# Optimization experiments

Measured on AMD Instinct MI355X. Metric: run time of the kernel, lower is better.

## Reference

```python
import jax, jax.numpy as jnp
import numpy as np

N, D = 8192, 32
SIGMA = 4.0
DAMPING = 0.5
MAX_ITER = 10
SHIFT_TOL = 1e-4


def _sqdist(a, b):
    # squared euclidean distances, (Na, Nb)
    sq = jnp.sum(a * a, axis=1)[:, None] + jnp.sum(b * b, axis=1)[None, :] - 2.0 * (a @ b.T)
    return jnp.maximum(sq, 0.0)


def setup_inputs() -> dict:
    key = jax.random.key(0)
    x = jax.random.normal(key, (N, D), dtype=jnp.float32)
    sigma = jnp.asarray(SIGMA, dtype=jnp.float32)  # learned scalar nn.Parameter
    return {"x": x, "sigma": sigma}


def _find_centroids(x, sigma):
    gamma = 1.0 / (2.0 * sigma ** 2)

    def body(carry, _):
        centroids, done = carry
        sq = _sqdist(x, centroids)              # (N, N); cdist(x,c)**2
        w = jnp.exp(-sq * gamma)                # gaussian kernel weights
        new_c = (w @ x) / jnp.sum(w, axis=1, keepdims=True)
        shift = jnp.linalg.norm(new_c - centroids, axis=1)
        # torch breaks BEFORE the damping update when max shift < tol
        done_new = done | (jnp.max(shift) < SHIFT_TOL)
        centroids = jnp.where(done_new, centroids,
                              DAMPING * centroids + (1.0 - DAMPING) * new_c)
        return (centroids, done_new), None

    (centroids, _), _ = jax.lax.scan(jax.remat(body), (x, jnp.asarray(False)), None, length=MAX_ITER)
    return centroids


def _nms_keep(x, centroids, threshold):
    n = centroids.shape[0]
    sq_pc = _sqdist(x, centroids)
    closest = jnp.argmin(sq_pc, axis=1)                      # (N,)
    scores = jnp.zeros((n,), jnp.int32).at[closest].add(1)   # counts per centroid
    sq_cc = _sqdist(centroids, centroids)
    overlap = (sq_cc < threshold ** 2) & ~jnp.eye(n, dtype=bool)
    order = jnp.argsort(-scores)                             # descending by score

    def body(keep, idx):
        active = keep[idx]
        keep2 = jnp.where(active, keep & ~overlap[idx], keep)
        keep2 = keep2.at[idx].set(jnp.where(active, scores[idx] > 0, keep2[idx]))
        return keep2, None

    keep, _ = jax.lax.scan(body, jnp.ones((n,), bool), order)
    return keep


def reference(x, sigma):
    centroids = _find_centroids(x, sigma)
    # threshold = sigma.item() in torch -> constant w.r.t. autodiff
    keep = _nms_keep(x, centroids, jax.lax.stop_gradient(sigma))
    # assignment over kept centroids only (dropped centroids get -inf cost -> 0 prob)
    cost = -jnp.sqrt(_sqdist(x, centroids) + 1e-12)
    cost = jnp.where(keep[None, :], cost, -jnp.inf)
    assignment = jax.nn.softmax(cost, axis=1)  # alpha == 1 branch
    return centroids, assignment, keep
```

## Files before the change

### kernel.cpp

```cpp
#include <hip/hip_runtime.h>
#include <math.h>

#define NPTS 8192
#define DIM 32
#define MAX_ITER 10
#define TOL 1e-4f
#define DAMP 0.5f

#define OFF_MSP   0u
#define OFF_CCUR  8650752u
#define OFF_CNEW  8912896u
#define OFF_NX    9175040u
#define OFF_NC    9183232u
#define OFF_PV    9191424u
#define OFF_PJ    9453568u
#define OFF_RKP   9715712u
#define OFF_PM    9977856u
#define OFF_PS   10240000u
#define OFF_MSH  10502144u
#define OFF_SCO  10502208u
#define OFF_ORD  10510400u

__global__ __launch_bounds__(256) void k_init(const float* __restrict__ x,
                                              float* __restrict__ c0,
                                              float* __restrict__ nx,
                                              float* __restrict__ nc) {
    int p = blockIdx.x * blockDim.x + threadIdx.x;
    const float4* xr = (const float4*)(x + (size_t)p * DIM);
    float4* cr = (float4*)(c0 + (size_t)p * DIM);
    float s = 0.f;
#pragma unroll
    for (int q = 0; q < 8; ++q) {
        float4 v = xr[q];
        cr[q] = v;
        s += v.x * v.x + v.y * v.y + v.z * v.z + v.w * v.w;
    }
    nx[p] = s;
    nc[p] = s;
}

__global__ __launch_bounds__(256) void k_ms2(const float* __restrict__ x,
                                             const float* __restrict__ nx,
                                             const float* __restrict__ c,
                                             const float* __restrict__ nc,
                                             const float* __restrict__ sigma_p,
                                             float* __restrict__ P) {
    int t = threadIdx.x;
    int wv = __builtin_amdgcn_readfirstlane(t >> 6);
    int lane = t & 63;
    int it = (int)blockIdx.x >> 5, js = (int)blockIdx.x & 31;
    int i = it * 256 + wv * 64 + lane;

    float sg = sigma_p[0];
    float gamma = 1.f / (2.f * sg * sg);

    float xi[DIM];
    const float4* xr = (const float4*)(x + (size_t)i * DIM);
#pragma unroll
    for (int q = 0; q < 8; ++q) {
        float4 v = xr[q];
        xi[4 * q] = v.x; xi[4 * q + 1] = v.y; xi[4 * q + 2] = v.z; xi[4 * q + 3] = v.w;
    }
    float nxi = nx[i];

    float acc[DIM];
#pragma unroll
    for (int d = 0; d < DIM; ++d) acc[d] = 0.f;
    float wsum = 0.f;

    int j0 = js * 256;
    const float* cb = c + (size_t)j0 * DIM;
    const float* xb = x + (size_t)j0 * DIM;
    const float* ncb = nc + j0;

    for (int jj = 0; jj < 256; ++jj) {
        const float4* cr = (const float4*)(cb + (size_t)jj * DIM);
        const float4* xr2 = (const float4*)(xb + (size_t)jj * DIM);
        float4 C[8], X[8];
#pragma unroll
        for (int q = 0; q < 8; ++q) C[q] = cr[q];
#pragma unroll
        for (int q = 0; q < 8; ++q) X[q] = xr2[q];
        float ncj = ncb[jj];
        float d0 = 0.f, d1 = 0.f, d2 = 0.f, d3 = 0.f;
#pragma unroll
        for (int q = 0; q < 8; ++q) {
            d0 = fmaf(xi[4 * q + 0], C[q].x, d0);
            d1 = fmaf(xi[4 * q + 1], C[q].y, d1);
            d2 = fmaf(xi[4 * q + 2], C[q].z, d2);
            d3 = fmaf(xi[4 * q + 3], C[q].w, d3);
        }
        float sq = fmaxf(nxi + ncj - 2.f * ((d0 + d1) + (d2 + d3)), 0.f);
        float w = __expf(-sq * gamma);
        wsum += w;
#pragma unroll
        for (int q = 0; q < 8; ++q) {
            acc[4 * q + 0] = fmaf(w, X[q].x, acc[4 * q + 0]);
            acc[4 * q + 1] = fmaf(w, X[q].y, acc[4 * q + 1]);
            acc[4 * q + 2] = fmaf(w, X[q].z, acc[4 * q + 2]);
            acc[4 * q + 3] = fmaf(w, X[q].w, acc[4 * q + 3]);
        }
    }

    size_t base = ((size_t)js * 33) * NPTS + i;
#pragma unroll
    for (int d = 0; d < DIM; ++d) P[base + (size_t)d * NPTS] = acc[d];
    P[base + (size_t)32 * NPTS] = wsum;
}

__global__ __launch_bounds__(256) void k_reduce(const float* __restrict__ P,
                                                const float* __restrict__ c_cur,
                                                float* __restrict__ c_new,
                                                unsigned int* __restrict__ maxshift) {
    int i = blockIdx.x * 256 + threadIdx.x;
    float tot[33];
#pragma unroll
    for (int d = 0; d < 33; ++d) tot[d] = 0.f;
    for (int js = 0; js < 32; ++js) {
        size_t base = ((size_t)js * 33) * NPTS + i;
#pragma unroll
        for (int d = 0; d < 33; ++d) tot[d] += P[base + (size_t)d * NPTS];
    }
    float ws = tot[32];
    const float* co = c_cur + (size_t)i * DIM;
    float sh2 = 0.f;
    float ncv[DIM];
#pragma unroll
    for (int d = 0; d < DIM; ++d) {
        float v = tot[d] / ws;
        ncv[d] = v;
        float df = v - co[d];
        sh2 = fmaf(df, df, sh2);
    }
    float4* dst = (float4*)(c_new + (size_t)i * DIM);
#pragma unroll
    for (int q = 0; q < 8; ++q)
        dst[q] = make_float4(ncv[4 * q], ncv[4 * q + 1], ncv[4 * q + 2], ncv[4 * q + 3]);
    atomicMax(maxshift, __float_as_uint(sqrtf(sh2)));
}

__global__ __launch_bounds__(256) void k_update(float* __restrict__ c_cur,
                                                const float* __restrict__ c_new,
                                                float* __restrict__ nc,
                                                const unsigned int* __restrict__ maxshift) {
    if (__uint_as_float(*maxshift) < TOL) return;
    int i = blockIdx.x * 256 + threadIdx.x;
    float4* cc = (float4*)(c_cur + (size_t)i * DIM);
    const float4* cn = (const float4*)(c_new + (size_t)i * DIM);
    float s = 0.f;
#pragma unroll
    for (int q = 0; q < 8; ++q) {
        float4 a = cc[q], b = cn[q];
        float4 r = make_float4(DAMP * a.x + (1.f - DAMP) * b.x,
                               DAMP * a.y + (1.f - DAMP) * b.y,
                               DAMP * a.z + (1.f - DAMP) * b.z,
                               DAMP * a.w + (1.f - DAMP) * b.w);
        cc[q] = r;
        s += r.x * r.x + r.y * r.y + r.z * r.z + r.w * r.w;
    }
    nc[i] = s;
}

__global__ __launch_bounds__(256) void k_scores2(const float* __restrict__ x,
                                                 const float* __restrict__ nx,
                                                 const float* __restrict__ c,
                                                 const float* __restrict__ nc,
                                                 float* __restrict__ pv,
                                                 int* __restrict__ pj) {
    int t = threadIdx.x;
    int wv = __builtin_amdgcn_readfirstlane(t >> 6);
    int lane = t & 63;
    int it = (int)blockIdx.x >> 5, js = (int)blockIdx.x & 31;
    int p = it * 256 + wv * 64 + lane;

    float xi[DIM];
    const float4* xr = (const float4*)(x + (size_t)p * DIM);
#pragma unroll
    for (int q = 0; q < 8; ++q) {
        float4 v = xr[q];
        xi[4 * q] = v.x; xi[4 * q + 1] = v.y; xi[4 * q + 2] = v.z; xi[4 * q + 3] = v.w;
    }
    float nxp = nx[p];

    int j0 = js * 256;
    const float* cb = c + (size_t)j0 * DIM;
    const float* ncb = nc + j0;
    float bestv = INFINITY;
    int bestj = j0;
    for (int jj = 0; jj < 256; ++jj) {
        const float4* cr = (const float4*)(cb + (size_t)jj * DIM);
        float4 C[8];
#pragma unroll
        for (int q = 0; q < 8; ++q) C[q] = cr[q];
        float d0 = 0.f, d1 = 0.f, d2 = 0.f, d3 = 0.f;
#pragma unroll
        for (int q = 0; q < 8; ++q) {
            d0 = fmaf(xi[4 * q + 0], C[q].x, d0);
            d1 = fmaf(xi[4 * q + 1], C[q].y, d1);
            d2 = fmaf(xi[4 * q + 2], C[q].z, d2);
            d3 = fmaf(xi[4 * q + 3], C[q].w, d3);
        }
        float sq = fmaxf(nxp + ncb[jj] - 2.f * ((d0 + d1) + (d2 + d3)), 0.f);
        if (sq < bestv) { bestv = sq; bestj = j0 + jj; }
    }
    pv[(size_t)js * NPTS + p] = bestv;
    pj[(size_t)js * NPTS + p] = bestj;
}

__global__ __launch_bounds__(256) void k_score_comb(const float* __restrict__ pv,
                                                    const int* __restrict__ pj,
                                                    int* __restrict__ scores) {
    int p = blockIdx.x * 256 + threadIdx.x;
    float bv = pv[p];
    int bj = pj[p];
    for (int js = 1; js < 32; ++js) {
        float v = pv[(size_t)js * NPTS + p];
        int j = pj[(size_t)js * NPTS + p];
        if (v < bv) { bv = v; bj = j; }
    }
    atomicAdd(&scores[bj], 1);
}

__global__ __launch_bounds__(256) void k_rank_part(const int* __restrict__ scores,
                                                   int* __restrict__ rkp) {
    int t = threadIdx.x;
    int wv = __builtin_amdgcn_readfirstlane(t >> 6);
    int lane = t & 63;
    int it = (int)blockIdx.x >> 5, js = (int)blockIdx.x & 31;
    int p = it * 256 + wv * 64 + lane;
    int sp = scores[p];
    int j0 = js * 256;
    int r = 0;
    for (int jj = 0; jj < 256; ++jj) {
        int sj = scores[j0 + jj];
        int j = j0 + jj;
        r += (sj > sp) || (sj == sp && j < p);
    }
    rkp[(size_t)js * NPTS + p] = r;
}

__global__ __launch_bounds__(256) void k_rank_comb(const int* __restrict__ rkp,
                                                   int* __restrict__ order) {
    int p = blockIdx.x * 256 + threadIdx.x;
    int r = 0;
    for (int js = 0; js < 32; ++js) r += rkp[(size_t)js * NPTS + p];
    order[r] = p;
}

__global__ __launch_bounds__(1024) void k_nms(const float* __restrict__ c,
                                              const int* __restrict__ order,
                                              const int* __restrict__ scores,
                                              const float* __restrict__ sigma_p,
                                              float* __restrict__ keep_out) {
    __shared__ int s_ord[NPTS];
    __shared__ unsigned char kp[NPTS];
    __shared__ int s_first[16];
    __shared__ int s_next;
    int t = threadIdx.x;
    for (int q = t; q < NPTS; q += 1024) { s_ord[q] = order[q]; kp[q] = 1; }
    __syncthreads();
    float sg = sigma_p[0];
    float thr2 = sg * sg;

    int k = 0;
    while (k < NPTS) {
        int cand = k + t;
        bool hit = (cand < NPTS) && (kp[s_ord[cand]] != 0);
        unsigned long long b = __ballot(hit);
        int wave = t >> 6;
        if ((t & 63) == 0)
            s_first[wave] = b ? (k + (wave << 6) + (__ffsll((unsigned long long)b) - 1))
                              : 0x7fffffff;
        __syncthreads();
        if (t == 0) {
            int mn = s_first[0];
            for (int w2 = 1; w2 < 16; ++w2) mn = min(mn, s_first[w2]);
            s_next = mn;
        }
        __syncthreads();
        int kf = s_next;
        if (kf == 0x7fffffff) { k += 1024; continue; }

        int idx = s_ord[kf];
        float ci[DIM];
        const float4* cr = (const float4*)(c + (size_t)idx * DIM);
#pragma unroll
        for (int q = 0; q < 8; ++q) {
            float4 v = cr[q];
            ci[4 * q] = v.x; ci[4 * q + 1] = v.y; ci[4 * q + 2] = v.z; ci[4 * q + 3] = v.w;
        }
#pragma unroll
        for (int m2 = 0; m2 < 8; ++m2) {
            int j = t + m2 * 1024;
            const float4* cj = (const float4*)(c + (size_t)j * DIM);
            float sq = 0.f;
#pragma unroll
            for (int q = 0; q < 8; ++q) {
                float4 v = cj[q];
                float e0 = v.x - ci[4 * q], e1 = v.y - ci[4 * q + 1];
                float e2 = v.z - ci[4 * q + 2], e3 = v.w - ci[4 * q + 3];
                sq += e0 * e0 + e1 * e1 + e2 * e2 + e3 * e3;
            }
            if (j != idx && sq < thr2) kp[j] = 0;
        }
        __syncthreads();
        if (t == 0) kp[idx] = (scores[idx] > 0) ? 1 : 0;
        __syncthreads();
        k = kf + 1;
    }
    __syncthreads();
    for (int q = t; q < NPTS; q += 1024) keep_out[q] = kp[q] ? 1.0f : 0.0f;
}

__global__ __launch_bounds__(256) void k_apass1(const float* __restrict__ x,
                                                const float* __restrict__ nx,
                                                const float* __restrict__ c,
                                                const float* __restrict__ nc,
                                                const float* __restrict__ keepf,
                                                float* __restrict__ pm,
                                                float* __restrict__ ps) {
    int t = threadIdx.x;
    int wv = __builtin_amdgcn_readfirstlane(t >> 6);
    int lane = t & 63;
    int it = (int)blockIdx.x >> 5, js = (int)blockIdx.x & 31;
    int p = it * 256 + wv * 64 + lane;

    float xi[DIM];
    const float4* xr = (const float4*)(x + (size_t)p * DIM);
#pragma unroll
    for (int q = 0; q < 8; ++q) {
        float4 v = xr[q];
        xi[4 * q] = v.x; xi[4 * q + 1] = v.y; xi[4 * q + 2] = v.z; xi[4 * q + 3] = v.w;
    }
    float nxp = nx[p];

    int j0 = js * 256;
    const float* cb = c + (size_t)j0 * DIM;
    const float* ncb = nc + j0;
    const float* kb = keepf + j0;
    float m = -1e30f, S = 0.f;
    for (int jj = 0; jj < 256; ++jj) {
        const float4* cr = (const float4*)(cb + (size_t)jj * DIM);
        float4 C[8];
#pragma unroll
        for (int q = 0; q < 8; ++q) C[q] = cr[q];
        float d0 = 0.f, d1 = 0.f, d2 = 0.f, d3 = 0.f;
#pragma unroll
        for (int q = 0; q < 8; ++q) {
            d0 = fmaf(xi[4 * q + 0], C[q].x, d0);
            d1 = fmaf(xi[4 * q + 1], C[q].y, d1);
            d2 = fmaf(xi[4 * q + 2], C[q].z, d2);
            d3 = fmaf(xi[4 * q + 3], C[q].w, d3);
        }
        float sq = fmaxf(nxp + ncb[jj] - 2.f * ((d0 + d1) + (d2 + d3)), 0.f);
        float cost = -sqrtf(sq + 1e-12f);
        float ck = (kb[jj] > 0.5f) ? cost : -INFINITY;
        float mn = fmaxf(m, ck);
        S = S * __expf(m - mn) + __expf(ck - mn);
        m = mn;
    }
    pm[(size_t)js * NPTS + p] = m;
    ps[(size_t)js * NPTS + p] = S;
}

__global__ __launch_bounds__(256) void k_acomb(const float* __restrict__ pm,
                                               const float* __restrict__ ps,
                                               const float* __restrict__ nx,
                                               float* __restrict__ A) {
    int p = blockIdx.x * 256 + threadIdx.x;
    float M = -1e30f;
    for (int js = 0; js < 32; ++js) M = fmaxf(M, pm[(size_t)js * NPTS + p]);
    float SS = 0.f;
    for (int js = 0; js < 32; ++js)
        SS += ps[(size_t)js * NPTS + p] * __expf(pm[(size_t)js * NPTS + p] - M);
    float* row = A + (size_t)p * NPTS;
    row[8189] = nx[p];
    row[8190] = M;
    row[8191] = 1.f / SS;
}

__global__ __launch_bounds__(256) void k_apass2(const float* __restrict__ x,
                                                const float* __restrict__ c,
                                                const float* __restrict__ keepf,
                                                float* __restrict__ A) {
    __shared__ float sNX[16], sM[16], sI[16];
    int t = threadIdx.x;
    int wv = __builtin_amdgcn_readfirstlane(t >> 6);
    int lane = t & 63;
    int p0 = blockIdx.x * 16;
    if (t < 16) {
        const float* row = A + (size_t)(p0 + t) * NPTS;
        sNX[t] = row[8189];
        sM[t] = row[8190];
        sI[t] = row[8191];
    }
    __syncthreads();

    for (int ch = wv; ch < 128; ch += 4) {
        int j = ch * 64 + lane;
        float cj[DIM];
        const float4* cr = (const float4*)(c + (size_t)j * DIM);
        float ncj = 0.f;
#pragma unroll
        for (int q = 0; q < 8; ++q) {
            float4 v = cr[q];
            cj[4 * q] = v.x; cj[4 * q + 1] = v.y; cj[4 * q + 2] = v.z; cj[4 * q + 3] = v.w;
            ncj += v.x * v.x + v.y * v.y + v.z * v.z + v.w * v.w;
        }
        float kpj = keepf[j];
        for (int pp = 0; pp < 16; ++pp) {
            const float4* xrow = (const float4*)(x + (size_t)(p0 + pp) * DIM);
            float4 X[8];
#pragma unroll
            for (int q = 0; q < 8; ++q) X[q] = xrow[q];
            float nxp = sNX[pp], M = sM[pp], inv = sI[pp];
            float d0 = 0.f, d1 = 0.f, d2 = 0.f, d3 = 0.f;
#pragma unroll
            for (int q = 0; q < 8; ++q) {
                d0 = fmaf(cj[4 * q + 0], X[q].x, d0);
                d1 = fmaf(cj[4 * q + 1], X[q].y, d1);
                d2 = fmaf(cj[4 * q + 2], X[q].z, d2);
                d3 = fmaf(cj[4 * q + 3], X[q].w, d3);
            }
            float sq = fmaxf(nxp + ncj - 2.f * ((d0 + d1) + (d2 + d3)), 0.f);
            float cost = -sqrtf(sq + 1e-12f);
            float v = (kpj > 0.5f) ? __expf(cost - M) * inv : 0.f;
            A[(size_t)(p0 + pp) * NPTS + j] = v;
        }
    }
}

extern "C" void kernel_launch(void* const* d_in, const int* in_sizes, int n_in,
                              void* d_out, int out_size, void* d_ws, size_t ws_size,
                              hipStream_t stream) {
    const float* x = (const float*)d_in[0];
    const float* sigma = (const float*)d_in[1];

    float* out = (float*)d_out;
    float* OUT_C = out;
    float* A = out + (size_t)NPTS * DIM;
    float* OUT_K = A + (size_t)NPTS * NPTS;

    float* msP = A + OFF_MSP;
    float* c_cur = A + OFF_CCUR;
    float* c_new = A + OFF_CNEW;
    float* nx = A + OFF_NX;
    float* nc = A + OFF_NC;
    float* pv = A + OFF_PV;
    int* pj = (int*)(A + OFF_PJ);
    int* rkp = (int*)(A + OFF_RKP);
    float* pm = A + OFF_PM;
    float* ps = A + OFF_PS;
    unsigned int* maxshift = (unsigned int*)(A + OFF_MSH);
    int* scores = (int*)(A + OFF_SCO);
    int* order = (int*)(A + OFF_ORD);

    k_init<<<NPTS / 256, 256, 0, stream>>>(x, c_cur, nx, nc);
    for (int itr = 0; itr < MAX_ITER; ++itr) {
        hipMemsetAsync(maxshift, 0, sizeof(unsigned int), stream);
        k_ms2<<<1024, 256, 0, stream>>>(x, nx, c_cur, nc, sigma, msP);
        k_reduce<<<NPTS / 256, 256, 0, stream>>>(msP, c_cur, c_new, maxshift);
        k_update<<<NPTS / 256, 256, 0, stream>>>(c_cur, c_new, nc, maxshift);
    }
    hipMemcpyAsync(OUT_C, c_cur, (size_t)NPTS * DIM * sizeof(float),
                   hipMemcpyDeviceToDevice, stream);

    hipMemsetAsync(scores, 0, NPTS * sizeof(int), stream);
    k_scores2<<<1024, 256, 0, stream>>>(x, nx, OUT_C, nc, pv, pj);
    k_score_comb<<<NPTS / 256, 256, 0, stream>>>(pv, pj, scores);
    k_rank_part<<<1024, 256, 0, stream>>>(scores, rkp);
    k_rank_comb<<<NPTS / 256, 256, 0, stream>>>(rkp, order);
    k_nms<<<1, 1024, 0, stream>>>(OUT_C, order, scores, sigma, OUT_K);

    k_apass1<<<1024, 256, 0, stream>>>(x, nx, OUT_C, nc, OUT_K, pm, ps);
    k_acomb<<<NPTS / 256, 256, 0, stream>>>(pm, ps, nx, A);
    k_apass2<<<NPTS / 16, 256, 0, stream>>>(x, OUT_C, OUT_K, A);
}
```

Baseline: 1.888 ms.

## Register-block two points per thread, drop softmax max pass, retile assignment kernel

The mean-shift, argmin and softmax-sum kernels now handle two query points per thread, so each centroid row loaded is reused across two dot products, and grids are halved. The softmax max is dropped because costs are non-positive and bounded, which removes the online rescaling and the k_acomb kernel. The final pass now stages 128 points in shared memory and tiles over 256 centroids per block. Fast exp2, sqrt and rcp intrinsics replace the library calls, and the separate memsets are folded into k_init with a per-iteration maxshift slot. Risks include higher register pressure and possible underflow for far points when no max subtraction is done.

```diff
diff --git a/kernel.cpp b/kernel.cpp
--- a/kernel.cpp
+++ b/kernel.cpp
@@ -6,6 +6,7 @@
 #define MAX_ITER 10
 #define TOL 1e-4f
 #define DAMP 0.5f
+#define LOG2E 1.4426950408889634f
 
 #define OFF_MSP   0u
 #define OFF_CCUR  8650752u
@@ -15,16 +16,16 @@
 #define OFF_PV    9191424u
 #define OFF_PJ    9453568u
 #define OFF_RKP   9715712u
-#define OFF_PM    9977856u
-#define OFF_PS   10240000u
-#define OFF_MSH  10502144u
-#define OFF_SCO  10502208u
-#define OFF_ORD  10510400u
+#define OFF_MSH   9977856u
+#define OFF_SCO   9977872u
+#define OFF_ORD   9986064u
 
 __global__ __launch_bounds__(256) void k_init(const float* __restrict__ x,
                                               float* __restrict__ c0,
                                               float* __restrict__ nx,
-                                              float* __restrict__ nc) {
+                                              float* __restrict__ nc,
+                                              int* __restrict__ scores,
+                                              unsigned int* __restrict__ msh) {
     int p = blockIdx.x * blockDim.x + threadIdx.x;
     const float4* xr = (const float4*)(x + (size_t)p * DIM);
     float4* cr = (float4*)(c0 + (size_t)p * DIM);
@@ -37,75 +38,103 @@
     }
     nx[p] = s;
     nc[p] = s;
-}
-
-__global__ __launch_bounds__(256) void k_ms2(const float* __restrict__ x,
-                                             const float* __restrict__ nx,
-                                             const float* __restrict__ c,
-                                             const float* __restrict__ nc,
-                                             const float* __restrict__ sigma_p,
-                                             float* __restrict__ P) {
+    scores[p] = 0;
+    if (blockIdx.x == 0 && threadIdx.x < 16) msh[threadIdx.x] = 0u;
+}
+
+__global__ __launch_bounds__(256, 2) void k_ms2(const float* __restrict__ x,
+                                                const float* __restrict__ nx,
+                                                const float* __restrict__ c,
+                                                const float* __restrict__ nc,
+                                                const float* __restrict__ sigma_p,
+                                                float* __restrict__ P) {
     int t = threadIdx.x;
     int wv = __builtin_amdgcn_readfirstlane(t >> 6);
     int lane = t & 63;
     int it = (int)blockIdx.x >> 5, js = (int)blockIdx.x & 31;
-    int i = it * 256 + wv * 64 + lane;
+    int i0 = it * 512 + wv * 128 + lane;
+    int i1 = i0 + 64;
 
     float sg = sigma_p[0];
-    float gamma = 1.f / (2.f * sg * sg);
-
-    float xi[DIM];
-    const float4* xr = (const float4*)(x + (size_t)i * DIM);
-#pragma unroll
-    for (int q = 0; q < 8; ++q) {
-        float4 v = xr[q];
-        xi[4 * q] = v.x; xi[4 * q + 1] = v.y; xi[4 * q + 2] = v.z; xi[4 * q + 3] = v.w;
-    }
-    float nxi = nx[i];
-
-    float acc[DIM];
-#pragma unroll
-    for (int d = 0; d < DIM; ++d) acc[d] = 0.f;
-    float wsum = 0.f;
-
-    int j0 = js * 256;
-    const float* cb = c + (size_t)j0 * DIM;
-    const float* xb = x + (size_t)j0 * DIM;
-    const float* ncb = nc + j0;
+    float ng2 = -LOG2E / (2.f * sg * sg);
+
+    float xi0[DIM], xi1[DIM];
+    {
+        const float4* xr0 = (const float4*)(x + (size_t)i0 * DIM);
+        const float4* xr1 = (const float4*)(x + (size_t)i1 * DIM);
+#pragma unroll
+        for (int q = 0; q < 8; ++q) {
+            float4 a = xr0[q], b = xr1[q];
+            xi0[4 * q] = a.x; xi0[4 * q + 1] = a.y; xi0[4 * q + 2] = a.z; xi0[4 * q + 3] = a.w;
+            xi1[4 * q] = b.x; xi1[4 * q + 1] = b.y; xi1[4 * q + 2] = b.z; xi1[4 * q + 3] = b.w;
+        }
+    }
+    float nx0 = nx[i0], nx1 = nx[i1];
+
+    float acc0[DIM], acc1[DIM];
+#pragma unroll
+    for (int d = 0; d < DIM; ++d) { acc0[d] = 0.f; acc1[d] = 0.f; }
+    float ws0 = 0.f, ws1 = 0.f;
+
+    int jb = js * 256;
+    const float* cb = c + (size_t)jb * DIM;
+    const float* xb = x + (size_t)jb * DIM;
+    const float* ncb = nc + jb;
 
     for (int jj = 0; jj < 256; ++jj) {
-        const float4* cr = (const float4*)(cb + (size_t)jj * DIM);
-        const float4* xr2 = (const float4*)(xb + (size_t)jj * DIM);
-        float4 C[8], X[8];
-#pragma unroll
-        for (int q = 0; q < 8; ++q) C[q] = cr[q];
-#pragma unroll
-        for (int q = 0; q < 8; ++q) X[q] = xr2[q];
-        float ncj = ncb[jj];
-        float d0 = 0.f, d1 = 0.f, d2 = 0.f, d3 = 0.f;
-#pragma unroll
-        for (int q = 0; q < 8; ++q) {
-            d0 = fmaf(xi[4 * q + 0], C[q].x, d0);
-            d1 = fmaf(xi[4 * q + 1], C[q].y, d1);
-            d2 = fmaf(xi[4 * q + 2], C[q].z, d2);
-            d3 = fmaf(xi[4 * q + 3], C[q].w, d3);
-        }
-        float sq = fmaxf(nxi + ncj - 2.f * ((d0 + d1) + (d2 + d3)), 0.f);
-        float w = __expf(-sq * gamma);
-        wsum += w;
-#pragma unroll
-        for (int q = 0; q < 8; ++q) {
-            acc[4 * q + 0] = fmaf(w, X[q].x, acc[4 * q + 0]);
-            acc[4 * q + 1] = fmaf(w, X[q].y, acc[4 * q + 1]);
-            acc[4 * q + 2] = fmaf(w, X[q].z, acc[4 * q + 2]);
-            acc[4 * q + 3] = fmaf(w, X[q].w, acc[4 * q + 3]);
-        }
-    }
-
-    size_t base = ((size_t)js * 33) * NPTS + i;
-#pragma unroll
-    for (int d = 0; d < DIM; ++d) P[base + (size_t)d * NPTS] = acc[d];
-    P[base + (size_t)32 * NPTS] = wsum;
+        float w0, w1;
+        {
+            const float4* cr = (const float4*)(cb + (size_t)jj * DIM);
+            float4 C[8];
+#pragma unroll
+            for (int q = 0; q < 8; ++q) C[q] = cr[q];
+            float ncj = ncb[jj];
+            float a0 = 0.f, a1 = 0.f, a2 = 0.f, a3 = 0.f;
+            float b0 = 0.f, b1 = 0.f, b2 = 0.f, b3 = 0.f;
+#pragma unroll
+            for (int q = 0; q < 8; ++q) {
+                a0 = fmaf(xi0[4 * q + 0], C[q].x, a0);
+                a1 = fmaf(xi0[4 * q + 1], C[q].y, a1);
+                a2 = fmaf(xi0[4 * q + 2], C[q].z, a2);
+                a3 = fmaf(xi0[4 * q + 3], C[q].w, a3);
+                b0 = fmaf(xi1[4 * q + 0], C[q].x, b0);
+                b1 = fmaf(xi1[4 * q + 1], C[q].y, b1);
+                b2 = fmaf(xi1[4 * q + 2], C[q].z, b2);
+                b3 = fmaf(xi1[4 * q + 3], C[q].w, b3);
+            }
+            float sq0 = fmaxf(fmaf(-2.f, (a0 + a1) + (a2 + a3), nx0 + ncj), 0.f);
+            float sq1 = fmaxf(fmaf(-2.f, (b0 + b1) + (b2 + b3), nx1 + ncj), 0.f);
+            w0 = __builtin_amdgcn_exp2f(ng2 * sq0);
+            w1 = __builtin_amdgcn_exp2f(ng2 * sq1);
+        }
+        ws0 += w0; ws1 += w1;
+        {
+            const float4* xr2 = (const float4*)(xb + (size_t)jj * DIM);
+            float4 X[8];
+#pragma unroll
+            for (int q = 0; q < 8; ++q) X[q] = xr2[q];
+#pragma unroll
+            for (int q = 0; q < 8; ++q) {
+                acc0[4 * q + 0] = fmaf(w0, X[q].x, acc0[4 * q + 0]);
+                acc0[4 * q + 1] = fmaf(w0, X[q].y, acc0[4 * q + 1]);
+                acc0[4 * q + 2] = fmaf(w0, X[q].z, acc0[4 * q + 2]);
+                acc0[4 * q + 3] = fmaf(w0, X[q].w, acc0[4 * q + 3]);
+                acc1[4 * q + 0] = fmaf(w1, X[q].x, acc1[4 * q + 0]);
+                acc1[4 * q + 1] = fmaf(w1, X[q].y, acc1[4 * q + 1]);
+                acc1[4 * q + 2] = fmaf(w1, X[q].z, acc1[4 * q + 2]);
+                acc1[4 * q + 3] = fmaf(w1, X[q].w, acc1[4 * q + 3]);
+            }
+        }
+    }
+
+    size_t base = ((size_t)js * 33) * NPTS + i0;
+#pragma unroll
+    for (int d = 0; d < DIM; ++d) {
+        P[base + (size_t)d * NPTS] = acc0[d];
+        P[base + (size_t)d * NPTS + 64] = acc1[d];
+    }
+    P[base + (size_t)32 * NPTS] = ws0;
+    P[base + (size_t)32 * NPTS + 64] = ws1;
 }
 
 __global__ __launch_bounds__(256) void k_reduce(const float* __restrict__ P,
@@ -122,12 +151,14 @@
         for (int d = 0; d < 33; ++d) tot[d] += P[base + (size_t)d * NPTS];
     }
     float ws = tot[32];
+    float inv = __builtin_amdgcn_rcpf(ws);
+    inv = inv * (2.f - ws * inv);
     const float* co = c_cur + (size_t)i * DIM;
     float sh2 = 0.f;
     float ncv[DIM];
 #pragma unroll
     for (int d = 0; d < DIM; ++d) {
-        float v = tot[d] / ws;
+        float v = tot[d] * inv;
         ncv[d] = v;
         float df = v - co[d];
         sh2 = fmaf(df, df, sh2);
@@ -136,7 +167,7 @@
 #pragma unroll
     for (int q = 0; q < 8; ++q)
         dst[q] = make_float4(ncv[4 * q], ncv[4 * q + 1], ncv[4 * q + 2], ncv[4 * q + 3]);
-    atomicMax(maxshift, __float_as_uint(sqrtf(sh2)));
+    atomicMax(maxshift, __float_as_uint(__builtin_amdgcn_sqrtf(sh2)));
 }
 
 __global__ __launch_bounds__(256) void k_update(float* __restrict__ c_cur,
@@ -161,50 +192,65 @@
     nc[i] = s;
 }
 
-__global__ __launch_bounds__(256) void k_scores2(const float* __restrict__ x,
-                                                 const float* __restrict__ nx,
-                                                 const float* __restrict__ c,
-                                                 const float* __restrict__ nc,
-                                                 float* __restrict__ pv,
-                                                 int* __restrict__ pj) {
+__global__ __launch_bounds__(256, 2) void k_scores2(const float* __restrict__ x,
+                                                    const float* __restrict__ nx,
+                                                    const float* __restrict__ c,
+                                                    const float* __restrict__ nc,
+                                                    float* __restrict__ pv,
+                                                    int* __restrict__ pj) {
     int t = threadIdx.x;
     int wv = __builtin_amdgcn_readfirstlane(t >> 6);
     int lane = t & 63;
     int it = (int)blockIdx.x >> 5, js = (int)blockIdx.x & 31;
-    int p = it * 256 + wv * 64 + lane;
-
-    float xi[DIM];
-    const float4* xr = (const float4*)(x + (size_t)p * DIM);
-#pragma unroll
-    for (int q = 0; q < 8; ++q) {
-        float4 v = xr[q];
-        xi[4 * q] = v.x; xi[4 * q + 1] = v.y; xi[4 * q + 2] = v.z; xi[4 * q + 3] = v.w;
-    }
-    float nxp = nx[p];
-
-    int j0 = js * 256;
-    const float* cb = c + (size_t)j0 * DIM;
-    const float* ncb = nc + j0;
-    float bestv = INFINITY;
-    int bestj = j0;
+    int p0 = it * 512 + wv * 128 + lane;
+    int p1 = p0 + 64;
+
+    float xi0[DIM], xi1[DIM];
+    {
+        const float4* xr0 = (const float4*)(x + (size_t)p0 * DIM);
+        const float4* xr1 = (const float4*)(x + (size_t)p1 * DIM);
+#pragma unroll
+        for (int q = 0; q < 8; ++q) {
+            float4 a = xr0[q], b = xr1[q];
+            xi0[4 * q] = a.x; xi0[4 * q + 1] = a.y; xi0[4 * q + 2] = a.z; xi0[4 * q + 3] = a.w;
+            xi1[4 * q] = b.x; xi1[4 * q + 1] = b.y; xi1[4 * q + 2] = b.z; xi1[4 * q + 3] = b.w;
+        }
+    }
+    float nxp0 = nx[p0], nxp1 = nx[p1];
+
+    int jb = js * 256;
+    const float* cb = c + (size_t)jb * DIM;
+    const float* ncb = nc + jb;
+    float bv0 = INFINITY, bv1 = INFINITY;
+    int bj0 = jb, bj1 = jb;
     for (int jj = 0; jj < 256; ++jj) {
         const float4* cr = (const float4*)(cb + (size_t)jj * DIM);
         float4 C[8];
 #pragma unroll
         for (int q = 0; q < 8; ++q) C[q] = cr[q];
-        float d0 = 0.f, d1 = 0.f, d2 = 0.f, d3 = 0.f;
-#pragma unroll
-        for (int q = 0; q < 8; ++q) {
-            d0 = fmaf(xi[4 * q + 0], C[q].x, d0);
-            d1 = fmaf(xi[4 * q + 1], C[q].y, d1);
-            d2 = fmaf(xi[4 * q + 2], C[q].z, d2);
-            d3 = fmaf(xi[4 * q + 3], C[q].w, d3);
-        }
-        float sq = fmaxf(nxp + ncb[jj] - 2.f * ((d0 + d1) + (d2 + d3)), 0.f);
-        if (sq < bestv) { bestv = sq; bestj = j0 + jj; }
-    }
-    pv[(size_t)js * NPTS + p] = bestv;
-    pj[(size_t)js * NPTS + p] = bestj;
+        float ncj = ncb[jj];
+        float a0 = 0.f, a1 = 0.f, a2 = 0.f, a3 = 0.f;
+        float b0 = 0.f, b1 = 0.f, b2 = 0.f, b3 = 0.f;
+#pragma unroll
+        for (int q = 0; q < 8; ++q) {
+            a0 = fmaf(xi0[4 * q + 0], C[q].x, a0);
+            a1 = fmaf(xi0[4 * q + 1], C[q].y, a1);
+            a2 = fmaf(xi0[4 * q + 2], C[q].z, a2);
+            a3 = fmaf(xi0[4 * q + 3], C[q].w, a3);
+            b0 = fmaf(xi1[4 * q + 0], C[q].x, b0);
+            b1 = fmaf(xi1[4 * q + 1], C[q].y, b1);
+            b2 = fmaf(xi1[4 * q + 2], C[q].z, b2);
+            b3 = fmaf(xi1[4 * q + 3], C[q].w, b3);
+        }
+        float sq0 = fmaxf(fmaf(-2.f, (a0 + a1) + (a2 + a3), nxp0 + ncj), 0.f);
+        float sq1 = fmaxf(fmaf(-2.f, (b0 + b1) + (b2 + b3), nxp1 + ncj), 0.f);
+        if (sq0 < bv0) { bv0 = sq0; bj0 = jb + jj; }
+        if (sq1 < bv1) { bv1 = sq1; bj1 = jb + jj; }
+    }
+    pv[(size_t)js * NPTS + p0] = bv0;
+    pj[(size_t)js * NPTS + p0] = bj0;
+    pv[(size_t)js * NPTS + p1] = bv1;
+    pj[(size_t)js * NPTS + p1] = bj1;
 }
 
 __global__ __launch_bounds__(256) void k_score_comb(const float* __restrict__ pv,
@@ -312,121 +358,134 @@
     for (int q = t; q < NPTS; q += 1024) keep_out[q] = kp[q] ? 1.0f : 0.0f;
 }
 
-__global__ __launch_bounds__(256) void k_apass1(const float* __restrict__ x,
-                                                const float* __restrict__ nx,
-                                                const float* __restrict__ c,
-                                                const float* __restrict__ nc,
-                                                const float* __restrict__ keepf,
-                                                float* __restrict__ pm,
-                                                float* __restrict__ ps) {
+__global__ __launch_bounds__(256, 2) void k_apass1(const float* __restrict__ x,
+                                                   const float* __restrict__ nx,
+                                                   const float* __restrict__ c,
+                                                   const float* __restrict__ nc,
+                                                   const float* __restrict__ keepf,
+                                                   float* __restrict__ ps) {
     int t = threadIdx.x;
     int wv = __builtin_amdgcn_readfirstlane(t >> 6);
     int lane = t & 63;
     int it = (int)blockIdx.x >> 5, js = (int)blockIdx.x & 31;
-    int p = it * 256 + wv * 64 + lane;
-
-    float xi[DIM];
-    const float4* xr = (const float4*)(x + (size_t)p * DIM);
-#pragma unroll
-    for (int q = 0; q < 8; ++q) {
-        float4 v = xr[q];
-        xi[4 * q] = v.x; xi[4 * q + 1] = v.y; xi[4 * q + 2] = v.z; xi[4 * q + 3] = v.w;
-    }
-    float nxp = nx[p];
-
-    int j0 = js * 256;
-    const float* cb = c + (size_t)j0 * DIM;
-    const float* ncb = nc + j0;
-    const float* kb = keepf + j0;
-    float m = -1e30f, S = 0.f;
+    int p0 = it * 512 + wv * 128 + lane;
+    int p1 = p0 + 64;
+
+    float xi0[DIM], xi1[DIM];
+    {
+        const float4* xr0 = (const float4*)(x + (size_t)p0 * DIM);
+        const float4* xr1 = (const float4*)(x + (size_t)p1 * DIM);
+#pragma unroll
+        for (int q = 0; q < 8; ++q) {
+            float4 a = xr0[q], b = xr1[q];
+            xi0[4 * q] = a.x; xi0[4 * q + 1] = a.y; xi0[4 * q + 2] = a.z; xi0[4 * q + 3] = a.w;
+            xi1[4 * q] = b.x; xi1[4 * q + 1] = b.y; xi1[4 * q + 2] = b.z; xi1[4 * q + 3] = b.w;
+        }
+    }
+    float nxp0 = nx[p0], nxp1 = nx[p1];
+
+    int jb = js * 256;
+    const float* cb = c + (size_t)jb * DIM;
+    const float* ncb = nc + jb;
+    const float* kb = keepf + jb;
+    float S0 = 0.f, S1 = 0.f;
     for (int jj = 0; jj < 256; ++jj) {
         const float4* cr = (const float4*)(cb + (size_t)jj * DIM);
         float4 C[8];
 #pragma unroll
         for (int q = 0; q < 8; ++q) C[q] = cr[q];
-        float d0 = 0.f, d1 = 0.f, d2 = 0.f, d3 = 0.f;
-#pragma unroll
-        for (int q = 0; q < 8; ++q) {
-            d0 = fmaf(xi[4 * q + 0], C[q].x, d0);
-            d1 = fmaf(xi[4 * q + 1], C[q].y, d1);
-            d2 = fmaf(xi[4 * q + 2], C[q].z, d2);
-            d3 = fmaf(xi[4 * q + 3], C[q].w, d3);
-        }
-        float sq = fmaxf(nxp + ncb[jj] - 2.f * ((d0 + d1) + (d2 + d3)), 0.f);
-        float cost = -sqrtf(sq + 1e-12f);
-        float ck = (kb[jj] > 0.5f) ? cost : -INFINITY;
-        float mn = fmaxf(m, ck);
-        S = S * __expf(m - mn) + __expf(ck - mn);
-        m = mn;
-    }
-    pm[(size_t)js * NPTS + p] = m;
-    ps[(size_t)js * NPTS + p] = S;
-}
-
-__global__ __launch_bounds__(256) void k_acomb(const float* __restrict__ pm,
-                                               const float* __restrict__ ps,
-                                               const float* __restrict__ nx,
-                                               float* __restrict__ A) {
-    int p = blockIdx.x * 256 + threadIdx.x;
-    float M = -1e30f;
-    for (int js = 0; js < 32; ++js) M = fmaxf(M, pm[(size_t)js * NPTS + p]);
-    float SS = 0.f;
-    for (int js = 0; js < 32; ++js)
-        SS += ps[(size_t)js * NPTS + p] * __expf(pm[(size_t)js * NPTS + p] - M);
-    float* row = A + (size_t)p * NPTS;
-    row[8189] = nx[p];
-    row[8190] = M;
-    row[8191] = 1.f / SS;
-}
-
-__global__ __launch_bounds__(256) void k_apass2(const float* __restrict__ x,
-                                                const float* __restrict__ c,
-                                                const float* __restrict__ keepf,
-                                                float* __restrict__ A) {
-    __shared__ float sNX[16], sM[16], sI[16];
+        float ncj = ncb[jj];
+        float kadd = (kb[jj] > 0.5f) ? 0.f : -1e38f;
+        float a0 = 0.f, a1 = 0.f, a2 = 0.f, a3 = 0.f;
+        float b0 = 0.f, b1 = 0.f, b2 = 0.f, b3 = 0.f;
+#pragma unroll
+        for (int q = 0; q < 8; ++q) {
+            a0 = fmaf(xi0[4 * q + 0], C[q].x, a0);
+            a1 = fmaf(xi0[4 * q + 1], C[q].y, a1);
+            a2 = fmaf(xi0[4 * q + 2], C[q].z, a2);
+            a3 = fmaf(xi0[4 * q + 3], C[q].w, a3);
+            b0 = fmaf(xi1[4 * q + 0], C[q].x, b0);
+            b1 = fmaf(xi1[4 * q + 1], C[q].y, b1);
+            b2 = fmaf(xi1[4 * q + 2], C[q].z, b2);
+            b3 = fmaf(xi1[4 * q + 3], C[q].w, b3);
+        }
+        float sq0 = fmaxf(fmaf(-2.f, (a0 + a1) + (a2 + a3), nxp0 + ncj), 0.f);
+        float sq1 = fmaxf(fmaf(-2.f, (b0 + b1) + (b2 + b3), nxp1 + ncj), 0.f);
+        float r0 = __builtin_amdgcn_sqrtf(sq0 + 1e-12f);
+        float r1 = __builtin_amdgcn_sqrtf(sq1 + 1e-12f);
+        S0 += __builtin_amdgcn_exp2f(fmaf(r0, -LOG2E, kadd));
+        S1 += __builtin_amdgcn_exp2f(fmaf(r1, -LOG2E, kadd));
+    }
+    ps[(size_t)js * NPTS + p0] = S0;
+    ps[(size_t)js * NPTS + p1] = S1;
+}
+
+__global__ __launch_bounds__(256, 4) void k_apass2(const float* __restrict__ x,
+                                                   const float* __restrict__ c,
+                                                   const float* __restrict__ keepf,
+                                                   const float* __restrict__ ps,
+                                                   float* __restrict__ A) {
+    __shared__ float sx[128 * 36];
+    __shared__ float snx[128];
+    __shared__ float sscale[128];
+    __shared__ float spart[256];
     int t = threadIdx.x;
     int wv = __builtin_amdgcn_readfirstlane(t >> 6);
     int lane = t & 63;
-    int p0 = blockIdx.x * 16;
-    if (t < 16) {
-        const float* row = A + (size_t)(p0 + t) * NPTS;
-        sNX[t] = row[8189];
-        sM[t] = row[8190];
-        sI[t] = row[8191];
+    int pt = (int)blockIdx.x >> 5, jt = (int)blockIdx.x & 31;
+    int p0 = pt * 128, j0 = jt * 256;
+
+    {
+        const float4* src = (const float4*)(x + (size_t)p0 * DIM) + t * 4;
+        int row = t >> 1, colh = (t & 1) * 16;
+        float4* dst = (float4*)(sx + row * 36 + colh);
+        float s = 0.f;
+#pragma unroll
+        for (int q = 0; q < 4; ++q) {
+            float4 v = src[q];
+            dst[q] = v;
+            s += v.x * v.x + v.y * v.y + v.z * v.z + v.w * v.w;
+        }
+        spart[t] = s;
     }
     __syncthreads();
-
-    for (int ch = wv; ch < 128; ch += 4) {
-        int j = ch * 64 + lane;
-        float cj[DIM];
+    if (t < 128) {
+        snx[t] = spart[2 * t] + spart[2 * t + 1];
+        float SS = 0.f;
+        for (int js = 0; js < 32; ++js) SS += ps[(size_t)js * NPTS + p0 + t];
+        sscale[t] = 1.f / SS;
+    }
+
+    int j = j0 + wv * 64 + lane;
+    float cj[DIM];
+    float ncj = 0.f;
+    {
         const float4* cr = (const float4*)(c + (size_t)j * DIM);
-        float ncj = 0.f;
 #pragma unroll
         for (int q = 0; q < 8; ++q) {
             float4 v = cr[q];
             cj[4 * q] = v.x; cj[4 * q + 1] = v.y; cj[4 * q + 2] = v.z; cj[4 * q + 3] = v.w;
             ncj += v.x * v.x + v.y * v.y + v.z * v.z + v.w * v.w;
         }
-        float kpj = keepf[j];
-        for (int pp = 0; pp < 16; ++pp) {
-            const float4* xrow = (const float4*)(x + (size_t)(p0 + pp) * DIM);
-            float4 X[8];
-#pragma unroll
-            for (int q = 0; q < 8; ++q) X[q] = xrow[q];
-            float nxp = sNX[pp], M = sM[pp], inv = sI[pp];
-            float d0 = 0.f, d1 = 0.f, d2 = 0.f, d3 = 0.f;
-#pragma unroll
-            for (int q = 0; q < 8; ++q) {
-                d0 = fmaf(cj[4 * q + 0], X[q].x, d0);
-                d1 = fmaf(cj[4 * q + 1], X[q].y, d1);
-                d2 = fmaf(cj[4 * q + 2], X[q].z, d2);
-                d3 = fmaf(cj[4 * q + 3], X[q].w, d3);
-            }
-            float sq = fmaxf(nxp + ncj - 2.f * ((d0 + d1) + (d2 + d3)), 0.f);
-            float cost = -sqrtf(sq + 1e-12f);
-            float v = (kpj > 0.5f) ? __expf(cost - M) * inv : 0.f;
-            A[(size_t)(p0 + pp) * NPTS + j] = v;
-        }
+    }
+    float kadd = (keepf[j] > 0.5f) ? 0.f : -1e38f;
+    __syncthreads();
+
+    for (int pp = 0; pp < 128; ++pp) {
+        const float4* xs = (const float4*)(sx + pp * 36);
+        float d0 = 0.f, d1 = 0.f, d2 = 0.f, d3 = 0.f;
+#pragma unroll
+        for (int q = 0; q < 8; ++q) {
+            float4 v = xs[q];
+            d0 = fmaf(cj[4 * q + 0], v.x, d0);
+            d1 = fmaf(cj[4 * q + 1], v.y, d1);
+            d2 = fmaf(cj[4 * q + 2], v.z, d2);
+            d3 = fmaf(cj[4 * q + 3], v.w, d3);
+        }
+        float sq = fmaxf(fmaf(-2.f, (d0 + d1) + (d2 + d3), snx[pp] + ncj), 0.f);
+        float rt = __builtin_amdgcn_sqrtf(sq + 1e-12f);
+        float tt = fmaf(rt, -LOG2E, kadd);
+        A[(size_t)(p0 + pp) * NPTS + j] = __builtin_amdgcn_exp2f(tt) * sscale[pp];
     }
 }
 
@@ -449,30 +508,26 @@
     float* pv = A + OFF_PV;
     int* pj = (int*)(A + OFF_PJ);
     int* rkp = (int*)(A + OFF_RKP);
-    float* pm = A + OFF_PM;
-    float* ps = A + OFF_PS;
-    unsigned int* maxshift = (unsigned int*)(A + OFF_MSH);
+    unsigned int* msh = (unsigned int*)(A + OFF_MSH);
     int* scores = (int*)(A + OFF_SCO);
     int* order = (int*)(A + OFF_ORD);
-
-    k_init<<<NPTS / 256, 256, 0, stream>>>(x, c_cur, nx, nc);
+    float* ps = (float*)d_ws;
+
+    k_init<<<NPTS / 256, 256, 0, stream>>>(x, c_cur, nx, nc, scores, msh);
     for (int itr = 0; itr < MAX_ITER; ++itr) {
-        hipMemsetAsync(maxshift, 0, sizeof(unsigned int), stream);
-        k_ms2<<<1024, 256, 0, stream>>>(x, nx, c_cur, nc, sigma, msP);
-        k_reduce<<<NPTS / 256, 256, 0, stream>>>(msP, c_cur, c_new, maxshift);
-        k_update<<<NPTS / 256, 256, 0, stream>>>(c_cur, c_new, nc, maxshift);
+        k_ms2<<<512, 256, 0, stream>>>(x, nx, c_cur, nc, sigma, msP);
+        k_reduce<<<NPTS / 256, 256, 0, stream>>>(msP, c_cur, c_new, msh + itr);
+        k_update<<<NPTS / 256, 256, 0, stream>>>(c_cur, c_new, nc, msh + itr);
     }
     hipMemcpyAsync(OUT_C, c_cur, (size_t)NPTS * DIM * sizeof(float),
                    hipMemcpyDeviceToDevice, stream);
 
-    hipMemsetAsync(scores, 0, NPTS * sizeof(int), stream);
-    k_scores2<<<1024, 256, 0, stream>>>(x, nx, OUT_C, nc, pv, pj);
+    k_scores2<<<512, 256, 0, stream>>>(x, nx, OUT_C, nc, pv, pj);
     k_score_comb<<<NPTS / 256, 256, 0, stream>>>(pv, pj, scores);
     k_rank_part<<<1024, 256, 0, stream>>>(scores, rkp);
     k_rank_comb<<<NPTS / 256, 256, 0, stream>>>(rkp, order);
     k_nms<<<1, 1024, 0, stream>>>(OUT_C, order, scores, sigma, OUT_K);
 
-    k_apass1<<<1024, 256, 0, stream>>>(x, nx, OUT_C, nc, OUT_K, pm, ps);
-    k_acomb<<<NPTS / 256, 256, 0, stream>>>(pm, ps, nx, A);
-    k_apass2<<<NPTS / 16, 256, 0, stream>>>(x, OUT_C, OUT_K, A);
-}
+    k_apass1<<<512, 256, 0, stream>>>(x, nx, OUT_C, nc, OUT_K, ps);
+    k_apass2<<<2048, 256, 0, stream>>>(x, OUT_C, OUT_K, ps, A);
+}
```

Result: faster. 1.822 ms (-3.5%).
